# Performance work log

Measured on AMD Instinct MI355X. Metric: run time of the kernel, lower is better.

Reference implementation:

```python
import jax, jax.numpy as jnp
import numpy as np

B, D, C = 4, 49, 512          # batch, tokens, in_features
N = 27                        # main nodes
NSUB = 14                     # sub nodes
C2 = C // 2                   # cross-attn q/k dim
BN_EPS = 1e-5
SCALE = C2 ** -0.5
# sub_list = [0,1,2,4,7,8,11]; each main node feeds two sub-sc rows
SUB_IDX = np.repeat(np.array([0, 1, 2, 4, 7, 8, 11]), 2)  # length 14


def _bn(x, w, b, axes):
    # training-mode batch norm (biased variance), matching nn.BatchNorm* forward math
    m = x.mean(axis=axes, keepdims=True)
    v = x.var(axis=axes, keepdims=True)
    return (x - m) * jax.lax.rsqrt(v + BN_EPS) * w + b


def _l2n(v):
    return v / jnp.maximum(jnp.linalg.norm(v, axis=-1, keepdims=True), 1e-12)


def setup_inputs() -> dict:
    key = jax.random.key(0)
    ks = iter(jax.random.split(key, 40))
    sC = float(np.sqrt(2.0 / C))
    sC2 = float(np.sqrt(2.0 / C2))
    W = lambda k, shape, sc: jax.random.normal(k, shape, jnp.float32) * sc
    inp = {}
    inp['x'] = jax.random.normal(next(ks), (B, D, C), jnp.float32)
    # 27 per-node LinearBlocks (fc + BN1d + relu), stacked
    inp['nb_W'] = W(next(ks), (N, C, C), sC)
    inp['nb_b'] = jnp.zeros((N, C), jnp.float32)
    inp['nb_bnw'] = jnp.ones((N, C), jnp.float32)
    inp['nb_bnb'] = jnp.zeros((N, C), jnp.float32)
    # FAM / ARM cross-attention params (torch Linear: [out,in] + bias)
    inp['fam_qW'] = W(next(ks), (C2, C), sC2); inp['fam_qb'] = jnp.zeros((C2,), jnp.float32)
    inp['fam_kW'] = W(next(ks), (C2, C), sC2); inp['fam_kb'] = jnp.zeros((C2,), jnp.float32)
    inp['fam_vW'] = W(next(ks), (C, C), sC);   inp['fam_vb'] = jnp.zeros((C,), jnp.float32)
    inp['arm_qW'] = W(next(ks), (C2, C), sC2); inp['arm_qb'] = jnp.zeros((C2,), jnp.float32)
    inp['arm_kW'] = W(next(ks), (C2, C), sC2); inp['arm_kb'] = jnp.zeros((C2,), jnp.float32)
    inp['arm_vW'] = W(next(ks), (C, C), sC);   inp['arm_vb'] = jnp.zeros((C,), jnp.float32)
    inp['ep_W'] = W(next(ks), (C, C), sC)
    inp['ep_b'] = jnp.zeros((C,), jnp.float32)
    inp['gem_bnw'] = jnp.ones((N * N,), jnp.float32)
    inp['gem_bnb'] = jnp.zeros((N * N,), jnp.float32)
    # 2 GatedGNN layers, 5 bias-free linears each
    inp['gnn_uW'] = W(next(ks), (2, C, C), sC)
    inp['gnn_vW'] = W(next(ks), (2, C, C), sC)
    inp['gnn_aW'] = W(next(ks), (2, C, C), sC)
    inp['gnn_bW'] = W(next(ks), (2, C, C), sC)
    inp['gnn_eW'] = W(next(ks), (2, C, C), sC)
    inp['gnn_bnvw'] = jnp.ones((2, N), jnp.float32)
    inp['gnn_bnvb'] = jnp.zeros((2, N), jnp.float32)
    inp['gnn_bnew'] = jnp.ones((2, N * N), jnp.float32)
    inp['gnn_bneb'] = jnp.zeros((2, N * N), jnp.float32)
    # similarity-calculation anchors (xavier-ish)
    inp['main_sc'] = W(next(ks), (N, C), float(np.sqrt(2.0 / (N + C))))
    inp['sub_sc'] = W(next(ks), (NSUB, C), float(np.sqrt(2.0 / (NSUB + C))))
    return inp


def _forward(x, nb_W, nb_b, nb_bnw, nb_bnb,
             fam_qW, fam_qb, fam_kW, fam_kb, fam_vW, fam_vb,
             arm_qW, arm_qb, arm_kW, arm_kb, arm_vW, arm_vb,
             ep_W, ep_b, gem_bnw, gem_bnb,
             gnn_uW, gnn_vW, gnn_aW, gnn_bW, gnn_eW,
             gnn_bnvw, gnn_bnvb, gnn_bnew, gnn_bneb,
             main_sc, sub_sc):
    # --- per-main-node LinearBlock, vmapped over the N node layers ---
    def node_block(W, b, bw, bb):
        h = x @ W.T + b                                   # [B,D,C]
        return jax.nn.relu(_bn(h, bw, bb, (0, 1)))        # BN1d over (batch, tokens)
    f_u = jax.vmap(node_block, in_axes=0, out_axes=1)(nb_W, nb_b, nb_bnw, nb_bnb)  # [B,N,D,C]
    f_v = f_u.mean(axis=2)                                # GAP -> [B,N,C]

    # --- GraphEdgeModel: FAM cross-attention (node tokens attend to global tokens) ---
    q = jnp.einsum('bndc,hc->bndh', f_u, fam_qW) + fam_qb # [B,N,D,C2]
    k = x @ fam_kW.T + fam_kb                             # [B,D,C2] (global feature = x, broadcast over N)
    v = x @ fam_vW.T + fam_vb                             # [B,D,C]
    attn = jax.nn.softmax(jnp.einsum('bndh,beh->bnde', q, k) * SCALE, axis=-1)
    feat = jnp.einsum('bnde,bec->bndc', attn, v)          # [B,N,D,C]

    # --- ARM cross-attention over all node pairs: edge e=i*N+j, query=feat[j] (start), key/value=feat[i] (end) ---
    Q = jnp.einsum('bndc,hc->bndh', feat, arm_qW) + arm_qb
    K = jnp.einsum('bndc,hc->bndh', feat, arm_kW) + arm_kb
    V = jnp.einsum('bndc,hc->bndh', feat, arm_vW) + arm_vb  # [B,N,D,C]
    dots = jnp.einsum('bjdh,bieh->bijde', Q, K) * SCALE     # [B,N,N,D,D]
    a2 = jax.nn.softmax(dots, axis=-1)
    fe = jnp.einsum('bijde,biec->bijdc', a2, V).reshape(B, N * N, D, C)

    edge = _bn(fe @ ep_W.T + ep_b,
               gem_bnw.reshape(1, -1, 1, 1), gem_bnb.reshape(1, -1, 1, 1), (0, 2, 3))
    f_e = edge.mean(axis=2).reshape(B, N, N, C)           # GAP over tokens -> [B,N,N,C]

    # --- 2 GatedGNN layers; start/end indicator einsums realized as broadcasts ---
    for l in range(2):
        res = f_v
        vi = f_v @ gnn_aW[l].T                            # end node i contribution
        vj = f_v @ gnn_bW[l].T                            # start node j contribution
        el = f_e @ gnn_eW[l].T
        m = vi[:, :, None, :] + vj[:, None, :, :] + el    # [B,N,N,C]
        m = _bn(m, gnn_bnew[l].reshape(1, N, N, 1), gnn_bneb[l].reshape(1, N, N, 1), (0, 3))
        f_e = f_e + jax.nn.relu(m)
        e = jax.nn.softmax(jax.nn.sigmoid(f_e), axis=2)   # softmax over start nodes j
        uj = f_v @ gnn_vW[l].T
        ui = f_v @ gnn_uW[l].T
        agg = ui + jnp.einsum('bijc,bjc->bic', e, uj) / N # scatter back to end node i
        f_v = res + jax.nn.relu(_bn(agg, gnn_bnvw[l].reshape(1, N, 1), gnn_bnvb[l].reshape(1, N, 1), (0, 2)))

    # --- SC layer: cosine similarity against relu+normalized anchors ---
    fvn = _l2n(f_v)
    main_cl = jnp.einsum('bnc,nc->bn', fvn, _l2n(jax.nn.relu(main_sc)))   # [B,27]
    sub_cl = jnp.einsum('bkc,kc->bk', fvn[:, SUB_IDX], _l2n(jax.nn.relu(sub_sc)))  # [B,14]
    return jnp.concatenate([main_cl, sub_cl], axis=-1)    # [B,41]


def reference(x, nb_W, nb_b, nb_bnw, nb_bnb,
              fam_qW, fam_qb, fam_kW, fam_kb, fam_vW, fam_vb,
              arm_qW, arm_qb, arm_kW, arm_kb, arm_vW, arm_vb,
              ep_W, ep_b, gem_bnw, gem_bnb,
              gnn_uW, gnn_vW, gnn_aW, gnn_bW, gnn_eW,
              gnn_bnvw, gnn_bnvb, gnn_bnew, gnn_bneb,
              main_sc, sub_sc):
    return _forward(x, nb_W, nb_b, nb_bnw, nb_bnb,
                    fam_qW, fam_qb, fam_kW, fam_kb, fam_vW, fam_vb,
                    arm_qW, arm_qb, arm_kW, arm_kb, arm_vW, arm_vb,
                    ep_W, ep_b, gem_bnw, gem_bnb,
                    gnn_uW, gnn_vW, gnn_aW, gnn_bW, gnn_eW,
                    gnn_bnvw, gnn_bnvb, gnn_bnew, gnn_bneb,
                    main_sc, sub_sc)
```

## Files before the change

### kernel.cpp

```cpp
#include <hip/hip_runtime.h>
#include <hip/hip_bf16.h>
#include <math.h>


namespace {

constexpr float SCALE_ = 0.0625f;
constexpr float EPS_   = 1e-5f;

typedef __attribute__((ext_vector_type(8))) short bf16x8;
typedef __attribute__((ext_vector_type(4))) short s16x4;
typedef __attribute__((ext_vector_type(4))) float f32x4;

__device__ __forceinline__ short f2bf(float f) {
  unsigned u = __float_as_uint(f);
  u += 0x7fffu + ((u >> 16) & 1u);
  return (short)(u >> 16);
}
__device__ __forceinline__ float bf2f(short h) {
  return __uint_as_float(((unsigned)(unsigned short)h) << 16);
}
__device__ __forceinline__ void split2(float f, short& h, short& l) {
  h = f2bf(f);
  l = f2bf(f - bf2f(h));
}

template<int CONVB>
__device__ __forceinline__
void gemm_bf3_core(const short* __restrict__ Ah, const short* __restrict__ Al,
                   const short* __restrict__ Wh, const short* __restrict__ Wl,
                   const float* __restrict__ Wf,
                   const float* __restrict__ bias, float* __restrict__ C,
                   short* __restrict__ Ch, short* __restrict__ Cl,
                   int M, int N, int K)
{
  __shared__ short sA[2][64][40];
  __shared__ short sB[2][64][40];
  const int tid  = threadIdx.x;
  const int n0   = blockIdx.x * 64, m0 = blockIdx.y * 64;
  const int wave = tid >> 6, lane = tid & 63;
  const int wr = (wave >> 1) * 32, wc = (wave & 1) * 32;
  const int lr = lane & 15, lk = (lane >> 4) * 8;
  const int sr = tid >> 2, sk = (tid & 3) * 8;
  const int arow = m0 + sr;

  f32x4 acc[2][2] = {};

  for (int k0 = 0; k0 < K; k0 += 32) {
    bf16x8 ah = {}, al = {};
    if (arow < M) {
      ah = *(const bf16x8*)(Ah + (long)arow * K + k0 + sk);
      al = *(const bf16x8*)(Al + (long)arow * K + k0 + sk);
    }
    bf16x8 bh, bl;
    if (CONVB) {
      f32x4 w0 = *(const f32x4*)(Wf + (long)(n0 + sr) * K + k0 + sk);
      f32x4 w1 = *(const f32x4*)(Wf + (long)(n0 + sr) * K + k0 + sk + 4);
#pragma unroll
      for (int j = 0; j < 4; ++j) {
        short h, l;
        split2(w0[j], h, l); bh[j] = h;     bl[j] = l;
        split2(w1[j], h, l); bh[4 + j] = h; bl[4 + j] = l;
      }
    } else {
      bh = *(const bf16x8*)(Wh + (long)(n0 + sr) * K + k0 + sk);
      bl = *(const bf16x8*)(Wl + (long)(n0 + sr) * K + k0 + sk);
    }
    __syncthreads();
    *(bf16x8*)&sA[0][sr][sk] = ah;
    *(bf16x8*)&sA[1][sr][sk] = al;
    *(bf16x8*)&sB[0][sr][sk] = bh;
    *(bf16x8*)&sB[1][sr][sk] = bl;
    __syncthreads();

    bf16x8 a0h = *(const bf16x8*)&sA[0][wr + lr][lk];
    bf16x8 a1h = *(const bf16x8*)&sA[0][wr + 16 + lr][lk];
    bf16x8 a0l = *(const bf16x8*)&sA[1][wr + lr][lk];
    bf16x8 a1l = *(const bf16x8*)&sA[1][wr + 16 + lr][lk];
    bf16x8 b0h = *(const bf16x8*)&sB[0][wc + lr][lk];
    bf16x8 b1h = *(const bf16x8*)&sB[0][wc + 16 + lr][lk];
    bf16x8 b0l = *(const bf16x8*)&sB[1][wc + lr][lk];
    bf16x8 b1l = *(const bf16x8*)&sB[1][wc + 16 + lr][lk];

    acc[0][0] = __builtin_amdgcn_mfma_f32_16x16x32_bf16(a0h, b0h, acc[0][0], 0, 0, 0);
    acc[0][1] = __builtin_amdgcn_mfma_f32_16x16x32_bf16(a0h, b1h, acc[0][1], 0, 0, 0);
    acc[1][0] = __builtin_amdgcn_mfma_f32_16x16x32_bf16(a1h, b0h, acc[1][0], 0, 0, 0);
    acc[1][1] = __builtin_amdgcn_mfma_f32_16x16x32_bf16(a1h, b1h, acc[1][1], 0, 0, 0);
    acc[0][0] = __builtin_amdgcn_mfma_f32_16x16x32_bf16(a0h, b0l, acc[0][0], 0, 0, 0);
    acc[0][1] = __builtin_amdgcn_mfma_f32_16x16x32_bf16(a0h, b1l, acc[0][1], 0, 0, 0);
    acc[1][0] = __builtin_amdgcn_mfma_f32_16x16x32_bf16(a1h, b0l, acc[1][0], 0, 0, 0);
    acc[1][1] = __builtin_amdgcn_mfma_f32_16x16x32_bf16(a1h, b1l, acc[1][1], 0, 0, 0);
    acc[0][0] = __builtin_amdgcn_mfma_f32_16x16x32_bf16(a0l, b0h, acc[0][0], 0, 0, 0);
    acc[0][1] = __builtin_amdgcn_mfma_f32_16x16x32_bf16(a0l, b1h, acc[0][1], 0, 0, 0);
    acc[1][0] = __builtin_amdgcn_mfma_f32_16x16x32_bf16(a1l, b0h, acc[1][0], 0, 0, 0);
    acc[1][1] = __builtin_amdgcn_mfma_f32_16x16x32_bf16(a1l, b1h, acc[1][1], 0, 0, 0);
  }

  const int rbase = m0 + wr + (lane >> 4) * 4;
  const int cb = n0 + wc + lr;
#pragma unroll
  for (int fj = 0; fj < 2; ++fj) {
    int col = cb + fj * 16;
    float bz = bias ? bias[col] : 0.f;
#pragma unroll
    for (int fi = 0; fi < 2; ++fi) {
#pragma unroll
      for (int r = 0; r < 4; ++r) {
        int row = rbase + fi * 16 + r;
        if (row < M) {
          float v = acc[fi][fj][r] + bz;
          long o = (long)row * N + col;
          if (C) C[o] = v;
          if (Ch) { short h, l; split2(v, h, l); Ch[o] = h; Cl[o] = l; }
        }
      }
    }
  }
}

template<int CONVB>
__global__ __launch_bounds__(256)
void gemm_bf3_k(const short* Ah, const short* Al, const short* Wh, const short* Wl,
                const float* Wf, const float* bias, float* C, short* Ch, short* Cl,
                int M, int N, int K, long aBS, long wBS, long bBS, long cBS)
{
  long z = blockIdx.z;
  gemm_bf3_core<CONVB>(Ah + z * aBS, Al + z * aBS,
                       Wh ? Wh + z * wBS : nullptr, Wl ? Wl + z * wBS : nullptr,
                       Wf ? Wf + z * wBS : nullptr,
                       bias ? bias + z * bBS : nullptr,
                       C ? C + z * cBS : nullptr,
                       Ch ? Ch + z * cBS : nullptr, Cl ? Cl + z * cBS : nullptr,
                       M, N, K);
}

struct G4 { const short* wh[4]; const short* wl[4]; float* c[4]; };

__global__ __launch_bounds__(256)
void gemm4_bf3_k(const short* Ah, const short* Al, G4 g, int M, int N, int K)
{
  int z = blockIdx.z;
  gemm_bf3_core<0>(Ah, Al, g.wh[z], g.wl[z], nullptr, nullptr, g.c[z],
                   nullptr, nullptr, M, N, K);
}

__global__ __launch_bounds__(256)
void cvt1_k(const float* __restrict__ s, short* __restrict__ dh,
            short* __restrict__ dl, int n4)
{
  long i = (long)blockIdx.x * 256 + threadIdx.x;
  if (i >= n4) return;
  f32x4 v = *(const f32x4*)(s + i * 4);
  s16x4 h, l;
#pragma unroll
  for (int j = 0; j < 4; ++j) { short hh, ll; split2(v[j], hh, ll); h[j] = hh; l[j] = ll; }
  *(s16x4*)(dh + i * 4) = h;
  *(s16x4*)(dl + i * 4) = l;
}

struct P10 { const float* s[10]; };

__global__ __launch_bounds__(256)
void cvt_w_k(P10 p, short* __restrict__ dh, short* __restrict__ dl)
{
  static const int tens[26] = {0,1,2,3,4,4,5,5,5,5,6,6,6,6,7,7,7,7,8,8,8,8,9,9,9,9};
  static const int coff[26] = {0,0,0,0,0,1,0,1,2,3,0,1,2,3,0,1,2,3,0,1,2,3,0,1,2,3};
  int c = blockIdx.y;
  const float* src = p.s[tens[c]] + (long)coff[c] * 131072;
  long dbase = (long)c * 131072;
  long i = ((long)blockIdx.x * 256 + threadIdx.x) * 8;
  f32x4 v0 = *(const f32x4*)(src + i);
  f32x4 v1 = *(const f32x4*)(src + i + 4);
  s16x4 h0, l0, h1, l1;
#pragma unroll
  for (int j = 0; j < 4; ++j) {
    short hh, ll;
    split2(v0[j], hh, ll); h0[j] = hh; l0[j] = ll;
    split2(v1[j], hh, ll); h1[j] = hh; l1[j] = ll;
  }
  *(s16x4*)(dh + dbase + i) = h0;     *(s16x4*)(dh + dbase + i + 4) = h1;
  *(s16x4*)(dl + dbase + i) = l0;     *(s16x4*)(dl + dbase + i + 4) = l1;
}

__global__ __launch_bounds__(256)
void gemm_nn_k(const float* __restrict__ A, const float* __restrict__ W,
               float* __restrict__ C, int M, int N, int K)
{
  __shared__ float As[32][68];
  __shared__ float Ws[32][68];
  const int tid = threadIdx.x;
  const int n0 = blockIdx.x * 64, m0 = blockIdx.y * 64;
  const int tx = tid & 15, ty = tid >> 4;
  float acc[4][4] = {};
  for (int k0 = 0; k0 < K; k0 += 32) {
#pragma unroll
    for (int p = 0; p < 2; ++p) {
      int idx = tid + p * 256;
      int row = idx >> 3, kq = idx & 7;
      float4 v = make_float4(0.f, 0.f, 0.f, 0.f);
      if (m0 + row < M)
        v = *(const float4*)(A + (long)(m0 + row) * K + k0 + kq * 4);
      As[kq*4+0][row] = v.x; As[kq*4+1][row] = v.y;
      As[kq*4+2][row] = v.z; As[kq*4+3][row] = v.w;
    }
#pragma unroll
    for (int p = 0; p < 2; ++p) {
      int idx = tid + p * 256;
      int row = idx >> 4, nq = idx & 15;
      float4 v = *(const float4*)(W + (long)(k0 + row) * N + n0 + nq * 4);
      *(float4*)&Ws[row][nq*4] = v;
    }
    __syncthreads();
#pragma unroll
    for (int k = 0; k < 32; ++k) {
      float4 a4 = *(const float4*)&As[k][ty*4];
      float4 b4 = *(const float4*)&Ws[k][tx*4];
      float av[4] = {a4.x, a4.y, a4.z, a4.w};
      float bv[4] = {b4.x, b4.y, b4.z, b4.w};
#pragma unroll
      for (int i2 = 0; i2 < 4; ++i2)
#pragma unroll
        for (int j2 = 0; j2 < 4; ++j2)
          acc[i2][j2] = fmaf(av[i2], bv[j2], acc[i2][j2]);
    }
    __syncthreads();
  }
#pragma unroll
  for (int i2 = 0; i2 < 4; ++i2) {
    int m = m0 + ty*4 + i2;
    if (m < M)
      *(float4*)(C + (long)m * N + n0 + tx*4) =
        make_float4(acc[i2][0], acc[i2][1], acc[i2][2], acc[i2][3]);
  }
}

__global__ __launch_bounds__(256)
void nb_stats(const float* __restrict__ H, float* __restrict__ mean, float* __restrict__ rs)
{
  int n = blockIdx.x;
  int c = blockIdx.y * 256 + threadIdx.x;
  const float* p = H + (long)n * 196 * 512 + c;
  float s = 0.f, q = 0.f;
  for (int r = 0; r < 196; ++r) { float v = p[(long)r * 512]; s += v; q = fmaf(v, v, q); }
  float m = s * (1.f / 196.f);
  float var = q * (1.f / 196.f) - m * m;
  mean[n * 512 + c] = m;
  rs[n * 512 + c] = rsqrtf(var + EPS_);
}

__global__ __launch_bounds__(256)
void nb_apply(const float* __restrict__ H, const float* __restrict__ mean,
              const float* __restrict__ rs, const float* __restrict__ bw,
              const float* __restrict__ bb,
              short* __restrict__ fuh, short* __restrict__ ful,
              float* __restrict__ fv, short* __restrict__ fvh, short* __restrict__ fvl)
{
  int n = blockIdx.x, b = blockIdx.y;
  int t = threadIdx.x;
#pragma unroll
  for (int cq = 0; cq < 2; ++cq) {
    int c = cq * 256 + t;
    float m = mean[n*512+c], r = rs[n*512+c];
    float w = bw[n*512+c], bias = bb[n*512+c];
    const float* hp = H + ((long)(n*4+b)*49) * 512 + c;
    long fo0 = ((long)(n*4+b)*49) * 512 + c;
    float s = 0.f;
    for (int d = 0; d < 49; ++d) {
      float v = hp[(long)d*512];
      float o = fmaxf(fmaf((v - m) * r, w, bias), 0.f);
      short hh, ll; split2(o, hh, ll);
      fuh[fo0 + (long)d*512] = hh;
      ful[fo0 + (long)d*512] = ll;
      s += o;
    }
    float fvv = s * (1.f / 49.f);
    long fo = ((long)b*27+n)*512 + c;
    fv[fo] = fvv;
    short hh, ll; split2(fvv, hh, ll);
    fvh[fo] = hh; fvl[fo] = ll;
  }
}

__global__ __launch_bounds__(512)
void attn_fam(const float* __restrict__ Qg, const float* __restrict__ Kg,
              const float* __restrict__ Vg, short* __restrict__ feath,
              short* __restrict__ featl)
{
  __shared__ float Qs[52][68];
  __shared__ float Ks[52][68];
  __shared__ float Ss[49][56];
  __shared__ float Vs[49][68];

  const int tid = threadIdx.x;
  const int bx = blockIdx.x, b = blockIdx.y;
  const int qblk = bx*4 + b;
  const long obase = ((long)b*1323 + (long)bx*49) * 512;
  const float* qp = Qg + (long)qblk * (49 * 256);
  const float* kp = Kg + (long)b * (49 * 256);
  const float* vp = Vg + (long)b * (49 * 512);

  const int tx = tid & 15;
  const int ty4 = tid >> 4;

  float sacc[2][4] = {};
  const int d0 = ty4 * 2;
  const int e0 = tx * 4;
  const int eh0 = (e0+0)&7, eh1 = (e0+1)&7, eh2 = (e0+2)&7, eh3 = (e0+3)&7;
  const int er0 = (e0+0) > 51 ? 51 : (e0+0);
  const int er1 = (e0+1) > 51 ? 51 : (e0+1);
  const int er2 = (e0+2) > 51 ? 51 : (e0+2);
  const int er3 = (e0+3) > 51 ? 51 : (e0+3);
  for (int kc = 0; kc < 256; kc += 64) {
    for (int idx = tid; idx < 49 * 16; idx += 512) {
      int row = idx >> 4, kq = idx & 15;
      *(float4*)&Qs[row][kq*4] = *(const float4*)(qp + (long)row*256 + kc + kq*4);
      *(float4*)&Ks[row][(kq ^ (row & 7)) * 4] = *(const float4*)(kp + (long)row*256 + kc + kq*4);
    }
    __syncthreads();
    if (d0 < 49) {
      const float* q0 = &Qs[d0][0];
      const float* q1 = &Qs[d0 + 1][0];
      const float* k0 = &Ks[er0][0];
      const float* k1 = &Ks[er1][0];
      const float* k2 = &Ks[er2][0];
      const float* k3 = &Ks[er3][0];
#pragma unroll 4
      for (int kq = 0; kq < 16; ++kq) {
        float4 a0 = *(const float4*)(q0 + kq*4);
        float4 a1 = *(const float4*)(q1 + kq*4);
        float4 b0 = *(const float4*)(k0 + ((kq ^ eh0) * 4));
        float4 b1 = *(const float4*)(k1 + ((kq ^ eh1) * 4));
        float4 b2 = *(const float4*)(k2 + ((kq ^ eh2) * 4));
        float4 b3 = *(const float4*)(k3 + ((kq ^ eh3) * 4));
        float av0[4] = {a0.x, a0.y, a0.z, a0.w};
        float av1[4] = {a1.x, a1.y, a1.z, a1.w};
        float bv[4][4] = {{b0.x,b0.y,b0.z,b0.w},{b1.x,b1.y,b1.z,b1.w},
                          {b2.x,b2.y,b2.z,b2.w},{b3.x,b3.y,b3.z,b3.w}};
#pragma unroll
        for (int j2 = 0; j2 < 4; ++j2) {
#pragma unroll
          for (int qq = 0; qq < 4; ++qq) {
            sacc[0][j2] = fmaf(av0[qq], bv[j2][qq], sacc[0][j2]);
            sacc[1][j2] = fmaf(av1[qq], bv[j2][qq], sacc[1][j2]);
          }
        }
      }
    }
    __syncthreads();
  }
  if (d0 < 49) {
#pragma unroll
    for (int i2 = 0; i2 < 2; ++i2) {
      int d = d0 + i2;
      if (d < 49) {
#pragma unroll
        for (int j2 = 0; j2 < 4; ++j2) {
          int e = e0 + j2;
          if (e < 49) Ss[d][e] = sacc[i2][j2] * SCALE_;
        }
      }
    }
  }
  __syncthreads();

  if (tid < 49) {
    float mx = -1e30f;
    for (int e = 0; e < 49; ++e) mx = fmaxf(mx, Ss[tid][e]);
    float sum = 0.f;
    for (int e = 0; e < 49; ++e) { float ex = __expf(Ss[tid][e] - mx); Ss[tid][e] = ex; sum += ex; }
    float inv = 1.f / sum;
    for (int e = 0; e < 49; ++e) Ss[tid][e] *= inv;
  }
  __syncthreads();

  const int td = ty4;
  const bool has2 = (td + 32) < 49;
  for (int cc = 0; cc < 512; cc += 64) {
    for (int idx = tid; idx < 49 * 16; idx += 512) {
      int row = idx >> 4, cq = idx & 15;
      *(float4*)&Vs[row][cq*4] = *(const float4*)(vp + (long)row*512 + cc + cq*4);
    }
    __syncthreads();
    float pa[2][4] = {};
#pragma unroll 7
    for (int e = 0; e < 49; ++e) {
      float4 v4 = *(const float4*)&Vs[e][tx*4];
      float p0 = Ss[td][e];
      float p1 = has2 ? Ss[td + 32][e] : 0.f;
      pa[0][0] = fmaf(p0, v4.x, pa[0][0]); pa[0][1] = fmaf(p0, v4.y, pa[0][1]);
      pa[0][2] = fmaf(p0, v4.z, pa[0][2]); pa[0][3] = fmaf(p0, v4.w, pa[0][3]);
      pa[1][0] = fmaf(p1, v4.x, pa[1][0]); pa[1][1] = fmaf(p1, v4.y, pa[1][1]);
      pa[1][2] = fmaf(p1, v4.z, pa[1][2]); pa[1][3] = fmaf(p1, v4.w, pa[1][3]);
    }
    __syncthreads();
    s16x4 hh, ll;
#pragma unroll
    for (int j = 0; j < 4; ++j) { short h, l; split2(pa[0][j], h, l); hh[j] = h; ll[j] = l; }
    *(s16x4*)(feath + obase + (long)td*512 + cc + tx*4) = hh;
    *(s16x4*)(featl + obase + (long)td*512 + cc + tx*4) = ll;
    if (has2) {
#pragma unroll
      for (int j = 0; j < 4; ++j) { short h, l; split2(pa[1][j], h, l); hh[j] = h; ll[j] = l; }
      *(s16x4*)(feath + obase + (long)(td+32)*512 + cc + tx*4) = hh;
      *(s16x4*)(featl + obase + (long)(td+32)*512 + cc + tx*4) = ll;
    }
  }
}

__global__ __launch_bounds__(512)
void bias2red_k(const float* __restrict__ epW, const float* __restrict__ vb,
                const float* __restrict__ epb, float* __restrict__ bias2,
                float* __restrict__ b2st)
{
  int c = threadIdx.x;
  float s = epb[c];
  const float* r = epW + (long)c * 512;
  for (int k = 0; k < 512; ++k) s = fmaf(r[k], vb[k], s);
  bias2[c] = s;
  __shared__ float red[16];
  float s1 = s, s2 = s * s;
#pragma unroll
  for (int off = 32; off; off >>= 1) { s1 += __shfl_down(s1, off); s2 += __shfl_down(s2, off); }
  int lane = c & 63, wid = c >> 6;
  if (lane == 0) { red[wid] = s1; red[8 + wid] = s2; }
  __syncthreads();
  if (c == 0) {
    float a = 0.f, qq = 0.f;
#pragma unroll
    for (int w = 0; w < 8; ++w) { a += red[w]; qq += red[8 + w]; }
    b2st[0] = a; b2st[1] = qq;
  }
}

__constant__ unsigned char TI_c[28] = {0,1,1,2,2,2,3,3,3,3,4,4,4,4,4,5,5,5,5,5,5,6,6,6,6,6,6,6};
__constant__ unsigned char TJ_c[28] = {0,0,1,0,1,2,0,1,2,3,0,1,2,3,4,0,1,2,3,4,5,0,1,2,3,4,5,6};

__global__ __launch_bounds__(256)
void gmat_k(const float* __restrict__ VW, const float* __restrict__ b2,
            float* __restrict__ G, float* __restrict__ V1, float* __restrict__ Vb2)
{
  __shared__ float Vs[49][260];
  const int i = blockIdx.x, b = blockIdx.y;
  const int tid = threadIdx.x;
  const int wave = tid >> 6, lane = tid & 63;
  const int di = lane >> 3, ej = lane & 7;
  const float* vp = VW + ((long)b*1323 + (long)i*49) * 512;
  float gacc[7];
#pragma unroll
  for (int t = 0; t < 7; ++t) gacc[t] = 0.f;
  float s1 = 0.f, s2 = 0.f;

  for (int half = 0; half < 2; ++half) {
    __syncthreads();
    for (int idx = tid; idx < 49 * 64; idx += 256) {
      int r = idx >> 6, q = idx & 63;
      *(float4*)&Vs[r][q*4] = *(const float4*)(vp + (long)r*512 + half*256 + q*4);
    }
    __syncthreads();
    int tt = 0;
    for (int t = wave; t < 28; t += 4, ++tt) {
      int d = TI_c[t]*8 + di, e = TJ_c[t]*8 + ej;
      int dc = d > 48 ? 48 : d, ec = e > 48 ? 48 : e;
      float g = gacc[tt];
      for (int q = 0; q < 64; ++q) {
        float4 a = *(const float4*)&Vs[dc][q*4];
        float4 bq = *(const float4*)&Vs[ec][q*4];
        g = fmaf(a.x, bq.x, fmaf(a.y, bq.y, fmaf(a.z, bq.z, fmaf(a.w, bq.w, g))));
      }
      gacc[tt] = g;
    }
    if (tid < 49) {
      for (int c = 0; c < 256; ++c) {
        float v = Vs[tid][c];
        s1 += v; s2 = fmaf(v, b2[half*256 + c], s2);
      }
    }
  }
  long gbase = ((long)b*27 + i) * 2401;
  int tt = 0;
  for (int t = wave; t < 28; t += 4, ++tt) {
    int ti = TI_c[t], tj = TJ_c[t];
    int d = ti*8 + di, e = tj*8 + ej;
    if (d < 49 && e < 49) {
      G[gbase + d*49 + e] = gacc[tt];
      if (ti != tj) G[gbase + e*49 + d] = gacc[tt];
    }
  }
  if (tid < 49) {
    long o = ((long)b*27 + i) * 49 + tid;
    V1[o] = s1; Vb2[o] = s2;
  }
}

__global__ __launch_bounds__(128)
void arm_post(const float* __restrict__ S, const float* __restrict__ G,
              const float* __restrict__ V1, const float* __restrict__ Vb2,
              float* __restrict__ Pbar, float* __restrict__ parts)
{
  __shared__ float TP[49 * 56];
  __shared__ float red[8];
  const int tid = threadIdx.x;
  const int x = blockIdx.x, b = blockIdx.y;
  const int i = x / 27, j = x - i * 27;
  const float* Sp = S + (long)b*1323*1344 + (long)j*49*1344 + (long)i*49;
  for (int idx = tid; idx < 2401; idx += 128) {
    unsigned d = ((unsigned)idx * 1338u) >> 16;
    unsigned e = (unsigned)idx - d * 49u;
    TP[d*56 + e] = Sp[(long)d*1344 + e];
  }
  for (int idx = tid; idx < 343; idx += 128) {
    int d = idx / 7, e = 49 + idx - d * 7;
    TP[d*56 + e] = 0.f;
  }
  __syncthreads();

  if (tid < 49) {
    float* pr = &TP[tid * 56];
    float mx = -1e30f;
    for (int e = 0; e < 49; ++e) mx = fmaxf(mx, pr[e]);
    float sum = 0.f;
    for (int e = 0; e < 49; ++e) { float ex = __expf(pr[e] - mx); pr[e] = ex; sum += ex; }
    float inv = 1.f / sum;
    for (int e = 0; e < 49; ++e) pr[e] *= inv;
  }
  __syncthreads();

  float lin = 0.f, pvb = 0.f;
  if (tid < 49) {
    float pb = 0.f;
    for (int d = 0; d < 49; ++d) pb += TP[d*56 + tid];
    Pbar[(((long)b*27 + i)*27 + j)*49 + tid] = pb;
    long vo = ((long)b*27 + i)*49 + tid;
    lin = pb * V1[vo];
    pvb = pb * Vb2[vo];
  }

  float q2 = 0.f;
  const float* Gp = G + ((long)b*27 + i) * 2401;
  for (int s = tid; s < 343; s += 128) {
    int k = s / 49;
    int e = s - k * 49;
    int k8 = k * 8;
    float t[8];
#pragma unroll
    for (int kk = 0; kk < 8; ++kk) t[kk] = 0.f;
#pragma unroll 7
    for (int d = 0; d < 49; ++d) {
      float pe = TP[d*56 + e];
      f32x4 a  = *(const f32x4*)&TP[d*56 + k8];
      f32x4 bq = *(const f32x4*)&TP[d*56 + k8 + 4];
      t[0] = fmaf(pe, a[0], t[0]); t[1] = fmaf(pe, a[1], t[1]);
      t[2] = fmaf(pe, a[2], t[2]); t[3] = fmaf(pe, a[3], t[3]);
      t[4] = fmaf(pe, bq[0], t[4]); t[5] = fmaf(pe, bq[1], t[5]);
      t[6] = fmaf(pe, bq[2], t[6]); t[7] = fmaf(pe, bq[3], t[7]);
    }
    const float* g = Gp + e * 49 + k8;
    int lim = 49 - k8;
#pragma unroll
    for (int kk = 0; kk < 8; ++kk)
      if (kk < lim) q2 = fmaf(t[kk], g[kk], q2);
  }

  float r1 = lin, r2 = q2 + 2.f * pvb;
#pragma unroll
  for (int off = 32; off; off >>= 1) { r1 += __shfl_down(r1, off); r2 += __shfl_down(r2, off); }
  int lane = tid & 63, wid = tid >> 6;
  if (lane == 0) { red[wid] = r1; red[2 + wid] = r2; }
  __syncthreads();
  if (tid == 0) {
    long o = ((long)b*729 + x) * 2;
    parts[o]     = red[0] + red[1];
    parts[o + 1] = red[2] + red[3];
  }
}

__global__ __launch_bounds__(256)
void edge_fin(const float* __restrict__ parts, const float* __restrict__ b2st,
              float* __restrict__ ems)
{
  int e = blockIdx.x * 256 + threadIdx.x;
  if (e < 729) {
    float B1 = b2st[0], nb2 = b2st[1];
    float s = 196.f * B1, q = 196.f * nb2;
#pragma unroll
    for (int b = 0; b < 4; ++b) {
      s += parts[((long)b * 729 + e) * 2 + 0];
      q += parts[((long)b * 729 + e) * 2 + 1];
    }
    const float inv = 1.f / 100352.f;
    float m = s * inv;
    float var = q * inv - m * m;
    ems[e*2]   = m;
    ems[e*2+1] = rsqrtf(var + EPS_);
  }
}

__global__ __launch_bounds__(256)
void fe_build(const float* __restrict__ Pbar, const float* __restrict__ VW,
              const float* __restrict__ b2, const float* __restrict__ ems,
              const float* __restrict__ gw, const float* __restrict__ gb,
              float* __restrict__ fe, short* __restrict__ feh, short* __restrict__ fel)
{
  __shared__ float Pb[27 * 49];
  const int i = blockIdx.x, b = blockIdx.y;
  const int tid = threadIdx.x;
  const float* pp = Pbar + ((long)b*27 + i) * 27 * 49;
  for (int idx = tid; idx < 1323; idx += 256) Pb[idx] = pp[idx];
  __syncthreads();
  const float* vp = VW + ((long)b*1323 + (long)i*49) * 512;
#pragma unroll 1
  for (int half = 0; half < 2; ++half) {
    int c = half * 256 + tid;
    float acc[27];
#pragma unroll
    for (int j = 0; j < 27; ++j) acc[j] = 0.f;
    for (int e = 0; e < 49; ++e) {
      float v = vp[(long)e*512 + c];
#pragma unroll
      for (int j = 0; j < 27; ++j) acc[j] = fmaf(Pb[j*49 + e], v, acc[j]);
    }
    float bz = b2[c];
#pragma unroll
    for (int j = 0; j < 27; ++j) {
      int ij = i*27 + j;
      float m = ems[ij*2], rs = ems[ij*2+1];
      float h = acc[j] * (1.f/49.f) + bz;
      float v = fmaf((h - m) * rs, gw[ij], gb[ij]);
      long o = ((long)b*729 + ij)*512 + c;
      fe[o] = v;
      short hh, ll; split2(v, hh, ll);
      feh[o] = hh; fel[o] = ll;
    }
  }
}

__global__ __launch_bounds__(256)
void gnn_edge_bn(const float* __restrict__ vi, const float* __restrict__ vj,
                 const float* __restrict__ el, const float* __restrict__ wv,
                 const float* __restrict__ bv, float* fe,
                 short* __restrict__ feh, short* __restrict__ fel)
{
  int ij = blockIdx.x; int i = ij / 27, j = ij - i * 27;
  int t = threadIdx.x;
  __shared__ float red[18];
  float mv[8]; float s = 0.f, q = 0.f;
#pragma unroll
  for (int p = 0; p < 8; ++p) {
    int idx = p * 256 + t; int b = idx >> 9, c = idx & 511;
    float v = vi[((long)b*27+i)*512 + c] + vj[((long)b*27+j)*512 + c]
            + el[((long)b*729+ij)*512 + c];
    mv[p] = v; s += v; q = fmaf(v, v, q);
  }
  int lane = t & 63, wid = t >> 6;
#pragma unroll
  for (int off = 32; off; off >>= 1) { s += __shfl_down(s, off); q += __shfl_down(q, off); }
  if (lane == 0) { red[wid] = s; red[4 + wid] = q; }
  __syncthreads();
  if (t == 0) {
    float S = red[0]+red[1]+red[2]+red[3], Q = red[4]+red[5]+red[6]+red[7];
    float m = S * (1.f / 2048.f);
    red[16] = m;
    red[17] = rsqrtf(Q * (1.f / 2048.f) - m * m + EPS_);
  }
  __syncthreads();
  float m = red[16], rs = red[17];
  float w = wv[ij], bb = bv[ij];
#pragma unroll
  for (int p = 0; p < 8; ++p) {
    int idx = p * 256 + t; int b = idx >> 9, c = idx & 511;
    long o = ((long)b*729+ij)*512 + c;
    float nv = fe[o] + fmaxf(fmaf((mv[p] - m) * rs, w, bb), 0.f);
    fe[o] = nv;
    short hh, ll; split2(nv, hh, ll);
    feh[o] = hh; fel[o] = ll;
  }
}

__global__ __launch_bounds__(256)
void gnn_agg(const float* __restrict__ fe, const float* __restrict__ ui,
             const float* __restrict__ uj, float* __restrict__ agg)
{
  int i = blockIdx.x, b = blockIdx.y;
  int t = threadIdx.x;
#pragma unroll
  for (int cq = 0; cq < 2; ++cq) {
    int c = cq * 256 + t;
    float sg[27];
    float mx = -1e30f;
#pragma unroll
    for (int j = 0; j < 27; ++j) {
      float x = fe[((long)b*729 + i*27 + j)*512 + c];
      float sgm = 1.f / (1.f + __expf(-x));
      sg[j] = sgm; mx = fmaxf(mx, sgm);
    }
    float sum = 0.f;
#pragma unroll
    for (int j = 0; j < 27; ++j) { float e2 = __expf(sg[j] - mx); sg[j] = e2; sum += e2; }
    float acc = 0.f;
#pragma unroll
    for (int j = 0; j < 27; ++j)
      acc = fmaf(sg[j], uj[((long)b*27+j)*512 + c], acc);
    agg[((long)b*27+i)*512 + c] = ui[((long)b*27+i)*512 + c] + acc / (sum * 27.f);
  }
}

__global__ __launch_bounds__(256)
void gnn_node_bn(const float* __restrict__ agg, const float* __restrict__ wv,
                 const float* __restrict__ bv, float* fv,
                 short* __restrict__ fvh, short* __restrict__ fvl)
{
  int i = blockIdx.x;
  int t = threadIdx.x;
  __shared__ float red[18];
  float mv[8]; float s = 0.f, q = 0.f;
#pragma unroll
  for (int p = 0; p < 8; ++p) {
    int idx = p * 256 + t; int b = idx >> 9, c = idx & 511;
    float v = agg[((long)b*27+i)*512 + c];
    mv[p] = v; s += v; q = fmaf(v, v, q);
  }
  int lane = t & 63, wid = t >> 6;
#pragma unroll
  for (int off = 32; off; off >>= 1) { s += __shfl_down(s, off); q += __shfl_down(q, off); }
  if (lane == 0) { red[wid] = s; red[4 + wid] = q; }
  __syncthreads();
  if (t == 0) {
    float S = red[0]+red[1]+red[2]+red[3], Q = red[4]+red[5]+red[6]+red[7];
    float m = S * (1.f / 2048.f);
    red[16] = m;
    red[17] = rsqrtf(Q * (1.f / 2048.f) - m * m + EPS_);
  }
  __syncthreads();
  float m = red[16], rs = red[17];
  float w = wv[i], bb = bv[i];
#pragma unroll
  for (int p = 0; p < 8; ++p) {
    int idx = p * 256 + t; int b = idx >> 9, c = idx & 511;
    long o = ((long)b*27+i)*512 + c;
    float nv = fv[o] + fmaxf(fmaf((mv[p] - m) * rs, w, bb), 0.f);
    fv[o] = nv;
    short hh, ll; split2(nv, hh, ll);
    fvh[o] = hh; fvl[o] = ll;
  }
}

__constant__ int SUB_IDX_c[14] = {0,0,1,1,2,2,4,4,7,7,8,8,11,11};

__global__ __launch_bounds__(64)
void sc_k(const float* __restrict__ fv, const float* __restrict__ mainsc,
          const float* __restrict__ subsc, float* __restrict__ out)
{
  int o = blockIdx.x, b = blockIdx.y;
  int lane = threadIdx.x;
  int r; const float* ap;
  if (o < 27) { r = o; ap = mainsc + (long)o * 512; }
  else        { int k = o - 27; r = SUB_IDX_c[k]; ap = subsc + (long)k * 512; }
  const float* fp = fv + ((long)b*27 + r) * 512;
  float sff = 0.f, saa = 0.f, sfa = 0.f;
  for (int c = lane; c < 512; c += 64) {
    float f = fp[c];
    float a = fmaxf(ap[c], 0.f);
    sff = fmaf(f, f, sff); saa = fmaf(a, a, saa); sfa = fmaf(f, a, sfa);
  }
#pragma unroll
  for (int off = 32; off; off >>= 1) {
    sff += __shfl_down(sff, off); saa += __shfl_down(saa, off); sfa += __shfl_down(sfa, off);
  }
  if (lane == 0)
    out[b * 41 + o] = sfa / (fmaxf(sqrtf(sff), 1e-12f) * fmaxf(sqrtf(saa), 1e-12f));
}

}

extern "C" void kernel_launch(void* const* d_in, const int* in_sizes, int n_in,
                              void* d_out, int out_size, void* d_ws, size_t ws_size,
                              hipStream_t stream)
{
  (void)in_sizes; (void)n_in; (void)out_size; (void)ws_size;
  const float* x       = (const float*)d_in[0];
  const float* nb_W    = (const float*)d_in[1];
  const float* nb_b    = (const float*)d_in[2];
  const float* nb_bnw  = (const float*)d_in[3];
  const float* nb_bnb  = (const float*)d_in[4];
  const float* fam_qW  = (const float*)d_in[5];
  const float* fam_qb  = (const float*)d_in[6];
  const float* fam_kW  = (const float*)d_in[7];
  const float* fam_kb  = (const float*)d_in[8];
  const float* fam_vW  = (const float*)d_in[9];
  const float* fam_vb  = (const float*)d_in[10];
  const float* arm_qW  = (const float*)d_in[11];
  const float* arm_qb  = (const float*)d_in[12];
  const float* arm_kW  = (const float*)d_in[13];
  const float* arm_kb  = (const float*)d_in[14];
  const float* arm_vW  = (const float*)d_in[15];
  const float* arm_vb  = (const float*)d_in[16];
  const float* ep_W    = (const float*)d_in[17];
  const float* ep_b    = (const float*)d_in[18];
  const float* gem_bnw = (const float*)d_in[19];
  const float* gem_bnb = (const float*)d_in[20];
  const float* gnn_uW  = (const float*)d_in[21];
  const float* gnn_vW  = (const float*)d_in[22];
  const float* gnn_aW  = (const float*)d_in[23];
  const float* gnn_bW  = (const float*)d_in[24];
  const float* gnn_eW  = (const float*)d_in[25];
  const float* gnn_bnvw = (const float*)d_in[26];
  const float* gnn_bnvb = (const float*)d_in[27];
  const float* gnn_bnew = (const float*)d_in[28];
  const float* gnn_bneb = (const float*)d_in[29];
  const float* main_sc  = (const float*)d_in[30];
  const float* sub_sc   = (const float*)d_in[31];
  float* out = (float*)d_out;

  char* wp = (char*)d_ws;
  auto carveF = [&](long n) -> float* { float* p = (float*)wp; wp += ((n + 15) & ~15L) * 4; return p; };
  auto carveS = [&](long n) -> short* { short* p = (short*)wp; wp += ((n + 15) & ~15L) * 2; return p; };

  float* Hnb   = carveF((long)27*196*512);
  float* S     = carveF((long)4*1323*1344);
  float* fe    = carveF((long)4*729*512);
  float* kf    = carveF(196*256);
  float* vf    = carveF(196*512);
  float* qfam  = carveF((long)5292*256);
  float* nbm   = carveF(27*512);
  float* nbr   = carveF(27*512);
  float* Mpre  = carveF(512*512);
  float* bias2 = carveF(512);
  float* b2st  = carveF(16);
  float* parts = carveF(4*729*2);
  float* ems   = carveF(1460);
  float* G     = carveF((long)108*2401);
  float* V1    = carveF(108*49);
  float* Vb2   = carveF(108*49);
  float* Pbar  = carveF((long)4*27*27*49);
  float* fv    = carveF(108*512);
  float* vi    = carveF(108*512);
  float* vj    = carveF(108*512);
  float* uj    = carveF(108*512);
  float* ui    = carveF(108*512);
  float* agg   = carveF(108*512);
  float* VW = Hnb;
  float* el = S;

  short* xh    = carveS(100352);
  short* xl    = carveS(100352);
  short* wph   = carveS((long)26*131072);
  short* wpl   = carveS((long)26*131072);
  short* Mpreh = carveS(262144);
  short* Mprel = carveS(262144);
  short* fuh   = carveS((long)5292*512);
  short* ful   = carveS((long)5292*512);
  short* Qah   = carveS((long)5292*256);
  short* Qal   = carveS((long)5292*256);
  short* Kah   = carveS((long)4*1344*256);
  short* Kal   = carveS((long)4*1344*256);
  short* fvh   = carveS(108*512);
  short* fvl   = carveS(108*512);
  short* feath = fuh;
  short* featl = ful;
  short* feh   = Qah;
  short* fel   = Kah;

  short* famqWh = wph + 0L*131072;        short* famqWl = wpl + 0L*131072;
  short* famkWh = wph + 1L*131072;        short* famkWl = wpl + 1L*131072;
  short* armqWh = wph + 2L*131072;        short* armqWl = wpl + 2L*131072;
  short* armkWh = wph + 3L*131072;        short* armkWl = wpl + 3L*131072;
  short* famvWh = wph + 4L*131072;        short* famvWl = wpl + 4L*131072;
  short* uWh    = wph + 6L*131072;        short* uWl    = wpl + 6L*131072;
  short* vWh    = wph + 10L*131072;       short* vWl    = wpl + 10L*131072;
  short* aWh    = wph + 14L*131072;       short* aWl    = wpl + 14L*131072;
  short* bWh    = wph + 18L*131072;       short* bWl    = wpl + 18L*131072;
  short* eWh    = wph + 22L*131072;       short* eWl    = wpl + 22L*131072;

  cvt1_k<<<dim3(98), 256, 0, stream>>>(x, xh, xl, 25088);
  P10 p10;
  p10.s[0] = fam_qW; p10.s[1] = fam_kW; p10.s[2] = arm_qW; p10.s[3] = arm_kW;
  p10.s[4] = fam_vW; p10.s[5] = gnn_uW; p10.s[6] = gnn_vW; p10.s[7] = gnn_aW;
  p10.s[8] = gnn_bW; p10.s[9] = gnn_eW;
  cvt_w_k<<<dim3(64, 26), 256, 0, stream>>>(p10, wph, wpl);

  gemm_bf3_k<1><<<dim3(8,4,27), 256, 0, stream>>>(xh, xl, nullptr, nullptr, nb_W,
      nb_b, Hnb, nullptr, nullptr, 196, 512, 512, 0, 262144, 512, 100352);
  nb_stats<<<dim3(27,2), 256, 0, stream>>>(Hnb, nbm, nbr);
  nb_apply<<<dim3(27,4), 256, 0, stream>>>(Hnb, nbm, nbr, nb_bnw, nb_bnb,
      fuh, ful, fv, fvh, fvl);
  gemm_bf3_k<0><<<dim3(4,4), 256, 0, stream>>>(xh, xl, famkWh, famkWl, nullptr,
      fam_kb, kf, nullptr, nullptr, 196, 256, 512, 0,0,0,0);
  gemm_bf3_k<0><<<dim3(8,4), 256, 0, stream>>>(xh, xl, famvWh, famvWl, nullptr,
      fam_vb, vf, nullptr, nullptr, 196, 512, 512, 0,0,0,0);
  gemm_bf3_k<0><<<dim3(4,83), 256, 0, stream>>>(fuh, ful, famqWh, famqWl, nullptr,
      fam_qb, qfam, nullptr, nullptr, 5292, 256, 512, 0,0,0,0);
  attn_fam<<<dim3(27,4), 512, 0, stream>>>(qfam, kf, vf, feath, featl);
  gemm_bf3_k<0><<<dim3(4,83), 256, 0, stream>>>(feath, featl, armqWh, armqWl, nullptr,
      arm_qb, nullptr, Qah, Qal, 5292, 256, 512, 0,0,0,0);
  gemm_bf3_k<0><<<dim3(4,21,4), 256, 0, stream>>>(feath, featl, armkWh, armkWl, nullptr,
      arm_kb, nullptr, Kah, Kal, 1323, 256, 512, (long)1323*512, 0, 0, (long)1344*256);
  gemm_nn_k<<<dim3(8,8), 256, 0, stream>>>(ep_W, arm_vW, Mpre, 512, 512, 512);
  cvt1_k<<<dim3(256), 256, 0, stream>>>(Mpre, Mpreh, Mprel, 65536);
  bias2red_k<<<dim3(1), 512, 0, stream>>>(ep_W, arm_vb, ep_b, bias2, b2st);
  gemm_bf3_k<0><<<dim3(8,83), 256, 0, stream>>>(feath, featl, Mpreh, Mprel, nullptr,
      nullptr, VW, nullptr, nullptr, 5292, 512, 512, 0,0,0,0);
  gemm_bf3_k<0><<<dim3(21,21,4), 256, 0, stream>>>(Qah, Qal, Kah, Kal, nullptr,
      nullptr, S, nullptr, nullptr, 1323, 1344, 256,
      (long)1323*256, (long)1344*256, 0, (long)1323*1344);
  gmat_k<<<dim3(27,4), 256, 0, stream>>>(VW, bias2, G, V1, Vb2);
  arm_post<<<dim3(729,4), 128, 0, stream>>>(S, G, V1, Vb2, Pbar, parts);
  edge_fin<<<dim3(3), 256, 0, stream>>>(parts, b2st, ems);
  fe_build<<<dim3(27,4), 256, 0, stream>>>(Pbar, VW, bias2, ems, gem_bnw, gem_bnb,
      fe, feh, fel);
  for (int l = 0; l < 2; ++l) {
    long wo = (long)l * 262144;
    G4 g4;
    g4.wh[0] = aWh + wo; g4.wl[0] = aWl + wo; g4.c[0] = vi;
    g4.wh[1] = bWh + wo; g4.wl[1] = bWl + wo; g4.c[1] = vj;
    g4.wh[2] = vWh + wo; g4.wl[2] = vWl + wo; g4.c[2] = uj;
    g4.wh[3] = uWh + wo; g4.wl[3] = uWl + wo; g4.c[3] = ui;
    gemm4_bf3_k<<<dim3(8,2,4), 256, 0, stream>>>(fvh, fvl, g4, 108, 512, 512);
    gemm_bf3_k<0><<<dim3(8,46), 256, 0, stream>>>(feh, fel, eWh + wo, eWl + wo, nullptr,
        nullptr, el, nullptr, nullptr, 2916, 512, 512, 0,0,0,0);
    gnn_edge_bn<<<dim3(729), 256, 0, stream>>>(vi, vj, el,
        gnn_bnew + (long)l*729, gnn_bneb + (long)l*729, fe, feh, fel);
    gnn_agg<<<dim3(27,4), 256, 0, stream>>>(fe, ui, uj, agg);
    gnn_node_bn<<<dim3(27), 256, 0, stream>>>(agg,
        gnn_bnvw + (long)l*27, gnn_bnvb + (long)l*27, fv, fvh, fvl);
  }
  sc_k<<<dim3(41,4), 64, 0, stream>>>(fv, main_sc, sub_sc, out);
}
```

Measured before the change: 655.3 us.

## Replace scalar FAM attention kernel with split-bf16 MFMA GEMMs plus softmax

Replaces the fp32 CUDA-core attn_fam kernel with three stages: a batched split-bf16 GEMM for Q·K^T into a padded 64-wide score buffer, a wave-level softmax kernel that writes P as hi/lo bf16, and a second batched GEMM P·V against a transposed, padded V. nb_apply now writes fu in batch-major layout, so the Q projection output lines up with the batched GEMM strides. The aim is to move the attention matmuls onto matrix cores. In exchange it adds extra launches, intermediate buffers and a V transpose kernel. It also aliases Kah/Kal and qfam as scratch, and the K buffer is only 49 rows per batch while the GEMM computes 64 columns.

```diff
diff --git a/kernel.cpp b/kernel.cpp
--- a/kernel.cpp
+++ b/kernel.cpp
@@ -263,7 +263,7 @@
     float m = mean[n*512+c], r = rs[n*512+c];
     float w = bw[n*512+c], bias = bb[n*512+c];
     const float* hp = H + ((long)(n*4+b)*49) * 512 + c;
-    long fo0 = ((long)(n*4+b)*49) * 512 + c;
+    long fo0 = ((long)b*1323 + (long)n*49) * 512 + c;
     float s = 0.f;
     for (int d = 0; d < 49; ++d) {
       float v = hp[(long)d*512];
@@ -281,129 +281,39 @@
   }
 }
 
-__global__ __launch_bounds__(512)
-void attn_fam(const float* __restrict__ Qg, const float* __restrict__ Kg,
-              const float* __restrict__ Vg, short* __restrict__ feath,
-              short* __restrict__ featl)
-{
-  __shared__ float Qs[52][68];
-  __shared__ float Ks[52][68];
-  __shared__ float Ss[49][56];
-  __shared__ float Vs[49][68];
-
-  const int tid = threadIdx.x;
-  const int bx = blockIdx.x, b = blockIdx.y;
-  const int qblk = bx*4 + b;
-  const long obase = ((long)b*1323 + (long)bx*49) * 512;
-  const float* qp = Qg + (long)qblk * (49 * 256);
-  const float* kp = Kg + (long)b * (49 * 256);
-  const float* vp = Vg + (long)b * (49 * 512);
-
-  const int tx = tid & 15;
-  const int ty4 = tid >> 4;
-
-  float sacc[2][4] = {};
-  const int d0 = ty4 * 2;
-  const int e0 = tx * 4;
-  const int eh0 = (e0+0)&7, eh1 = (e0+1)&7, eh2 = (e0+2)&7, eh3 = (e0+3)&7;
-  const int er0 = (e0+0) > 51 ? 51 : (e0+0);
-  const int er1 = (e0+1) > 51 ? 51 : (e0+1);
-  const int er2 = (e0+2) > 51 ? 51 : (e0+2);
-  const int er3 = (e0+3) > 51 ? 51 : (e0+3);
-  for (int kc = 0; kc < 256; kc += 64) {
-    for (int idx = tid; idx < 49 * 16; idx += 512) {
-      int row = idx >> 4, kq = idx & 15;
-      *(float4*)&Qs[row][kq*4] = *(const float4*)(qp + (long)row*256 + kc + kq*4);
-      *(float4*)&Ks[row][(kq ^ (row & 7)) * 4] = *(const float4*)(kp + (long)row*256 + kc + kq*4);
-    }
-    __syncthreads();
-    if (d0 < 49) {
-      const float* q0 = &Qs[d0][0];
-      const float* q1 = &Qs[d0 + 1][0];
-      const float* k0 = &Ks[er0][0];
-      const float* k1 = &Ks[er1][0];
-      const float* k2 = &Ks[er2][0];
-      const float* k3 = &Ks[er3][0];
-#pragma unroll 4
-      for (int kq = 0; kq < 16; ++kq) {
-        float4 a0 = *(const float4*)(q0 + kq*4);
-        float4 a1 = *(const float4*)(q1 + kq*4);
-        float4 b0 = *(const float4*)(k0 + ((kq ^ eh0) * 4));
-        float4 b1 = *(const float4*)(k1 + ((kq ^ eh1) * 4));
-        float4 b2 = *(const float4*)(k2 + ((kq ^ eh2) * 4));
-        float4 b3 = *(const float4*)(k3 + ((kq ^ eh3) * 4));
-        float av0[4] = {a0.x, a0.y, a0.z, a0.w};
-        float av1[4] = {a1.x, a1.y, a1.z, a1.w};
-        float bv[4][4] = {{b0.x,b0.y,b0.z,b0.w},{b1.x,b1.y,b1.z,b1.w},
-                          {b2.x,b2.y,b2.z,b2.w},{b3.x,b3.y,b3.z,b3.w}};
-#pragma unroll
-        for (int j2 = 0; j2 < 4; ++j2) {
-#pragma unroll
-          for (int qq = 0; qq < 4; ++qq) {
-            sacc[0][j2] = fmaf(av0[qq], bv[j2][qq], sacc[0][j2]);
-            sacc[1][j2] = fmaf(av1[qq], bv[j2][qq], sacc[1][j2]);
-          }
-        }
-      }
-    }
-    __syncthreads();
-  }
-  if (d0 < 49) {
-#pragma unroll
-    for (int i2 = 0; i2 < 2; ++i2) {
-      int d = d0 + i2;
-      if (d < 49) {
-#pragma unroll
-        for (int j2 = 0; j2 < 4; ++j2) {
-          int e = e0 + j2;
-          if (e < 49) Ss[d][e] = sacc[i2][j2] * SCALE_;
-        }
-      }
-    }
-  }
-  __syncthreads();
-
-  if (tid < 49) {
-    float mx = -1e30f;
-    for (int e = 0; e < 49; ++e) mx = fmaxf(mx, Ss[tid][e]);
-    float sum = 0.f;
-    for (int e = 0; e < 49; ++e) { float ex = __expf(Ss[tid][e] - mx); Ss[tid][e] = ex; sum += ex; }
-    float inv = 1.f / sum;
-    for (int e = 0; e < 49; ++e) Ss[tid][e] *= inv;
-  }
-  __syncthreads();
-
-  const int td = ty4;
-  const bool has2 = (td + 32) < 49;
-  for (int cc = 0; cc < 512; cc += 64) {
-    for (int idx = tid; idx < 49 * 16; idx += 512) {
-      int row = idx >> 4, cq = idx & 15;
-      *(float4*)&Vs[row][cq*4] = *(const float4*)(vp + (long)row*512 + cc + cq*4);
-    }
-    __syncthreads();
-    float pa[2][4] = {};
+__global__ __launch_bounds__(256)
+void sm_fam_k(const float* __restrict__ Sf, short* __restrict__ Ph,
+              short* __restrict__ Pl)
+{
+  int row = blockIdx.x * 4 + (threadIdx.x >> 6);
+  int e = threadIdx.x & 63;
+  float v = (e < 49) ? Sf[(long)row * 64 + e] * SCALE_ : -1e30f;
+  float mx = v;
+#pragma unroll
+  for (int off = 32; off; off >>= 1) mx = fmaxf(mx, __shfl_xor(mx, off));
+  float ex = (e < 49) ? __expf(v - mx) : 0.f;
+  float sum = ex;
+#pragma unroll
+  for (int off = 32; off; off >>= 1) sum += __shfl_xor(sum, off);
+  float p = ex / sum;
+  short h, l; split2(p, h, l);
+  Ph[(long)row * 64 + e] = h;
+  Pl[(long)row * 64 + e] = l;
+}
+
+__global__ __launch_bounds__(256)
+void vt_cvt_k(const float* __restrict__ vf, short* __restrict__ VTh,
+              short* __restrict__ VTl)
+{
+  int b = blockIdx.x;
+  int n = blockIdx.y * 256 + threadIdx.x;
+  long obase = ((long)b * 512 + n) * 64;
 #pragma unroll 7
-    for (int e = 0; e < 49; ++e) {
-      float4 v4 = *(const float4*)&Vs[e][tx*4];
-      float p0 = Ss[td][e];
-      float p1 = has2 ? Ss[td + 32][e] : 0.f;
-      pa[0][0] = fmaf(p0, v4.x, pa[0][0]); pa[0][1] = fmaf(p0, v4.y, pa[0][1]);
-      pa[0][2] = fmaf(p0, v4.z, pa[0][2]); pa[0][3] = fmaf(p0, v4.w, pa[0][3]);
-      pa[1][0] = fmaf(p1, v4.x, pa[1][0]); pa[1][1] = fmaf(p1, v4.y, pa[1][1]);
-      pa[1][2] = fmaf(p1, v4.z, pa[1][2]); pa[1][3] = fmaf(p1, v4.w, pa[1][3]);
-    }
-    __syncthreads();
-    s16x4 hh, ll;
-#pragma unroll
-    for (int j = 0; j < 4; ++j) { short h, l; split2(pa[0][j], h, l); hh[j] = h; ll[j] = l; }
-    *(s16x4*)(feath + obase + (long)td*512 + cc + tx*4) = hh;
-    *(s16x4*)(featl + obase + (long)td*512 + cc + tx*4) = ll;
-    if (has2) {
-#pragma unroll
-      for (int j = 0; j < 4; ++j) { short h, l; split2(pa[1][j], h, l); hh[j] = h; ll[j] = l; }
-      *(s16x4*)(feath + obase + (long)(td+32)*512 + cc + tx*4) = hh;
-      *(s16x4*)(featl + obase + (long)(td+32)*512 + cc + tx*4) = ll;
-    }
+  for (int k = 0; k < 64; ++k) {
+    float v = (k < 49) ? vf[((long)b * 49 + k) * 512 + n] : 0.f;
+    short h, l; split2(v, h, l);
+    VTh[obase + k] = h;
+    VTl[obase + k] = l;
   }
 }
 
@@ -840,6 +750,8 @@
   float* agg   = carveF(108*512);
   float* VW = Hnb;
   float* el = S;
+  float* Sfam = qfam;
+  (void)kf;
 
   short* xh    = carveS(100352);
   short* xl    = carveS(100352);
@@ -855,8 +767,14 @@
   short* Kal   = carveS((long)4*1344*256);
   short* fvh   = carveS(108*512);
   short* fvl   = carveS(108*512);
+  short* kfh   = carveS(212*256);
+  short* kfl   = carveS(212*256);
+  short* vth   = carveS((long)4*512*64);
+  short* vtl   = carveS((long)4*512*64);
   short* feath = fuh;
   short* featl = ful;
+  short* Pfh   = Kah;
+  short* Pfl   = Kal;
   short* feh   = Qah;
   short* fel   = Kah;
 
@@ -884,12 +802,19 @@
   nb_apply<<<dim3(27,4), 256, 0, stream>>>(Hnb, nbm, nbr, nb_bnw, nb_bnb,
       fuh, ful, fv, fvh, fvl);
   gemm_bf3_k<0><<<dim3(4,4), 256, 0, stream>>>(xh, xl, famkWh, famkWl, nullptr,
-      fam_kb, kf, nullptr, nullptr, 196, 256, 512, 0,0,0,0);
+      fam_kb, nullptr, kfh, kfl, 196, 256, 512, 0,0,0,0);
   gemm_bf3_k<0><<<dim3(8,4), 256, 0, stream>>>(xh, xl, famvWh, famvWl, nullptr,
       fam_vb, vf, nullptr, nullptr, 196, 512, 512, 0,0,0,0);
+  vt_cvt_k<<<dim3(4,2), 256, 0, stream>>>(vf, vth, vtl);
   gemm_bf3_k<0><<<dim3(4,83), 256, 0, stream>>>(fuh, ful, famqWh, famqWl, nullptr,
-      fam_qb, qfam, nullptr, nullptr, 5292, 256, 512, 0,0,0,0);
-  attn_fam<<<dim3(27,4), 512, 0, stream>>>(qfam, kf, vf, feath, featl);
+      fam_qb, nullptr, Qah, Qal, 5292, 256, 512, 0,0,0,0);
+  gemm_bf3_k<0><<<dim3(1,21,4), 256, 0, stream>>>(Qah, Qal, kfh, kfl, nullptr,
+      nullptr, Sfam, nullptr, nullptr, 1323, 64, 256,
+      (long)1323*256, (long)49*256, 0, (long)1323*64);
+  sm_fam_k<<<dim3(1323), 256, 0, stream>>>(Sfam, Pfh, Pfl);
+  gemm_bf3_k<0><<<dim3(8,21,4), 256, 0, stream>>>(Pfh, Pfl, vth, vtl, nullptr,
+      nullptr, nullptr, feath, featl, 1323, 512, 64,
+      (long)1323*64, (long)512*64, 0, (long)1323*512);
   gemm_bf3_k<0><<<dim3(4,83), 256, 0, stream>>>(feath, featl, armqWh, armqWl, nullptr,
       arm_qb, nullptr, Qah, Qal, 5292, 256, 512, 0,0,0,0);
   gemm_bf3_k<0><<<dim3(4,21,4), 256, 0, stream>>>(feath, featl, armkWh, armkWl, nullptr,
```

Result: no change. 645.5 us (-1.5%).
